# Kernel tuning notes

Hardware: AMD Instinct MI355X
Metric: run time of the kernel (lower is better)

Reference implementation:

```python
import jax, jax.numpy as jnp
import numpy as np

N_NODES = 100000

def setup_inputs() -> dict:
    key = jax.random.key(0)
    ks = jax.random.split(key, 8)
    n_feat, nhid, nclass = 256, 128, 40
    n_edges = 1600000
    x = jax.random.normal(ks[0], (N_NODES, n_feat), dtype=jnp.float32)
    edge_index = jax.random.randint(ks[1], (2, n_edges), 0, N_NODES, dtype=jnp.int64)
    # Glorot-ish scaled weights
    W1 = jax.random.normal(ks[2], (n_feat, nhid), dtype=jnp.float32) / np.sqrt(n_feat)
    b1 = jnp.zeros((nhid,), dtype=jnp.float32)
    W2 = jax.random.normal(ks[3], (nhid, nhid), dtype=jnp.float32) / np.sqrt(nhid)
    b2 = jnp.zeros((nhid,), dtype=jnp.float32)
    Wc = jax.random.normal(ks[4], (nhid, nclass), dtype=jnp.float32) / np.sqrt(nhid)
    bc = jnp.zeros((nclass,), dtype=jnp.float32)
    return {"x": x, "edge_index": edge_index, "W1": W1, "b1": b1,
            "W2": W2, "b2": b2, "Wc": Wc, "bc": bc}


def _gcn_conv(x, src, dst, W, b, n_nodes):
    """PyG GCNConv: transform, then sym-normalized aggregation with self-loops.
    out_i = sum_{j in N(i) u {i}} (d_i^-1/2 d_j^-1/2) (x_j W) + b,
    where d = in-degree over A + I.
    """
    h = x @ W  # [N, out]
    ones = jnp.ones_like(dst, dtype=h.dtype)
    deg = jax.ops.segment_sum(ones, dst, num_segments=n_nodes) + 1.0  # + self loop
    dinv = jax.lax.rsqrt(deg)  # deg >= 1, always valid
    norm = dinv[src] * dinv[dst]  # [E]
    msg = h[src] * norm[:, None]  # [E, out]  (dominant gather traffic)
    agg = jax.ops.segment_sum(msg, dst, num_segments=n_nodes)
    agg = agg + h * (dinv * dinv)[:, None]  # self-loop contribution
    return agg + b


def reference(x, edge_index, W1, b1, W2, b2, Wc, bc):
    # eval mode: dropout is identity
    src, dst = edge_index[0], edge_index[1]
    n = x.shape[0]
    h = jax.nn.relu(_gcn_conv(x, src, dst, W1, b1, n))
    h = jax.nn.relu(_gcn_conv(h, src, dst, W2, b2, n))
    return h @ Wc + bc
```

## Files before the change

### kernel.cpp

```cpp
#include <hip/hip_runtime.h>
#include <hip/hip_bf16.h>
#include <hip/hip_fp16.h>
#include <type_traits>


typedef _Float16 half8 __attribute__((ext_vector_type(8)));
typedef _Float16 half4v __attribute__((ext_vector_type(4)));
typedef float floatx4 __attribute__((ext_vector_type(4)));

#define EPB 8192


__device__ inline int block_incl_scan_256(int t, int* tmp) {
    int tid = threadIdx.x;
    tmp[tid] = t;
    __syncthreads();
    #pragma unroll
    for (int off = 1; off < 256; off <<= 1) {
        int v = (tid >= off) ? tmp[tid - off] : 0;
        __syncthreads();
        tmp[tid] += v;
        __syncthreads();
    }
    return tmp[tid];
}

template <int ITEMS>
__global__ __launch_bounds__(256) void k_scan1(const int* __restrict__ v,
                                               int* __restrict__ bsum, int n) {
    __shared__ int tmp[256];
    int base = blockIdx.x * (256 * ITEMS) + threadIdx.x * ITEMS;
    int t = 0;
    #pragma unroll
    for (int l = 0; l < ITEMS; ++l) {
        int i = base + l;
        t += (i < n) ? v[i] : 0;
    }
    block_incl_scan_256(t, tmp);
    if (threadIdx.x == 0) bsum[blockIdx.x] = tmp[255];
}

__global__ __launch_bounds__(256) void k_scan2(int* __restrict__ bsum, int nb) {
    __shared__ int tmp[256];
    int tid = threadIdx.x;
    int v = (tid < nb) ? bsum[tid] : 0;
    block_incl_scan_256(v, tmp);
    if (tid < nb) bsum[tid] = tid ? tmp[tid - 1] : 0;
}

template <int ITEMS>
__global__ __launch_bounds__(256) void k_scan3(const int* __restrict__ vin,
                                               const int* __restrict__ bsum,
                                               int* __restrict__ rp, int n) {
    __shared__ int tmp[256];
    int base = blockIdx.x * (256 * ITEMS) + threadIdx.x * ITEMS;
    int v[ITEMS];
    int t = 0;
    #pragma unroll
    for (int l = 0; l < ITEMS; ++l) {
        int i = base + l;
        v[l] = (i < n) ? vin[i] : 0;
        t += v[l];
    }
    block_incl_scan_256(t, tmp);
    int run = bsum[blockIdx.x] + (threadIdx.x ? tmp[threadIdx.x - 1] : 0);
    #pragma unroll
    for (int l = 0; l < ITEMS; ++l) {
        int i = base + l;
        if (i < n) rp[i] = run;
        run += v[l];
    }
}


__global__ __launch_bounds__(256) void k_histA(const int* __restrict__ dst,
                                               int* __restrict__ histM,
                                               int E, int nblk) {
    __shared__ int h[512];
    int tid = threadIdx.x;
    for (int i = tid; i < 512; i += 256) h[i] = 0;
    __syncthreads();
    int base = blockIdx.x * EPB;
    #pragma unroll 4
    for (int l = 0; l < EPB / 256; ++l) {
        int i = base + l * 256 + tid;
        if (i < E) atomicAdd(&h[dst[i] >> 8], 1);
    }
    __syncthreads();
    for (int i = tid; i < 512; i += 256)
        histM[i * nblk + blockIdx.x] = h[i];
}

__global__ __launch_bounds__(256) void k_scatterA(const int* __restrict__ src,
                                                  const int* __restrict__ dst,
                                                  const int* __restrict__ histS,
                                                  unsigned long long* __restrict__ eB,
                                                  int E, int nblk) {
    __shared__ int bse[512];
    __shared__ int cnt[512];
    int tid = threadIdx.x;
    for (int i = tid; i < 512; i += 256) {
        bse[i] = histS[i * nblk + blockIdx.x];
        cnt[i] = 0;
    }
    __syncthreads();
    int base = blockIdx.x * EPB;
    #pragma unroll 4
    for (int l = 0; l < EPB / 256; ++l) {
        int i = base + l * 256 + tid;
        if (i < E) {
            int d = dst[i];
            int s = src[i];
            int b = d >> 8;
            int r = atomicAdd(&cnt[b], 1);
            eB[bse[b] + r] = ((unsigned long long)(unsigned)d << 32) | (unsigned)s;
        }
    }
}

#define BCAP 4608
__global__ __launch_bounds__(256) void k_sortB(const unsigned long long* __restrict__ eB,
                                               const int* __restrict__ histS,
                                               int* __restrict__ srcS,
                                               int* __restrict__ rowptr,
                                               float* __restrict__ dinv,
                                               int n, int E, int nblk) {
    const int b   = blockIdx.x;
    const int tid = threadIdx.x;
    const int ni0 = b << 8;
    int s0 = histS[b * nblk];
    int s1 = (b < 511) ? histS[(b + 1) * nblk] : E;
    int cnt = s1 - s0;
    if (cnt > BCAP) cnt = BCAP;
    if (cnt == 0 && ni0 > n) return;

    __shared__ int hist[256];
    __shared__ int tmp[256];
    __shared__ int baseA[256];
    __shared__ int cntA[256];
    __shared__ int dstL[BCAP];
    __shared__ unsigned srcL[BCAP];
    __shared__ int lbA[256];

    hist[tid] = 0;
    cntA[tid] = 0;
    __syncthreads();
    for (int i = s0 + tid; i < s0 + cnt; i += 256) {
        int d = (int)(eB[i] >> 32);
        atomicAdd(&hist[d & 255], 1);
    }
    __syncthreads();
    int own  = hist[tid];
    int incl = block_incl_scan_256(own, tmp);
    baseA[tid] = incl - own;
    __syncthreads();
    for (int i = s0 + tid; i < s0 + cnt; i += 256) {
        unsigned long long v = eB[i];
        int d = (int)(v >> 32);
        int dig = d & 255;
        int r = atomicAdd(&cntA[dig], 1);
        int pos = baseA[dig] + r;
        dstL[pos] = d;
        srcL[pos] = (unsigned)v;
    }
    __syncthreads();
    for (int j = tid; j < cnt; j += 256)
        srcS[s0 + j] = (int)srcL[j];
    if (ni0 <= n) {
        int i = ni0 + tid;
        int lo = 0, hi = cnt;
        while (lo < hi) {
            int mid = (lo + hi) >> 1;
            if (dstL[mid] < i) lo = mid + 1; else hi = mid;
        }
        lbA[tid] = lo;
        __syncthreads();
        if (i <= n) {
            rowptr[i] = s0 + lo;
            if (i < n) {
                int ub = (tid < 255) ? lbA[tid + 1] : cnt;
                dinv[i] = rsqrtf((float)(ub - lo + 1));
            }
        }
    }
}

__global__ __launch_bounds__(256) void k_wcast(const float* __restrict__ W,
                                               _Float16* __restrict__ Wt,
                                               int N, int K, int kbits, int total) {
    int i = blockIdx.x * 256 + threadIdx.x;
    if (i < total) {
        int c = i >> kbits;
        int k = i & (K - 1);
        Wt[i] = (c < N) ? (_Float16)W[(size_t)k * N + c] : (_Float16)0.f;
    }
}


template <int K, int BN, int MT, typename AT, typename OT>
__global__ __launch_bounds__(256) void gemm_bres(const AT* __restrict__ A,
                                                 const _Float16* __restrict__ Wt,
                                                 const float* __restrict__ bias,
                                                 OT* __restrict__ C,
                                                 int M, int N) {
    constexpr int KP = K + 8;
    constexpr int NT = BN / 16;
    __shared__ __align__(16) _Float16 Bs[BN * KP];

    const int tid  = threadIdx.x;
    const int lane = tid & 63;
    const int wv   = tid >> 6;
    const int qd   = lane >> 4;
    const int ln15 = lane & 15;
    const int bm   = blockIdx.x * (64 * MT);

    constexpr int TOT = BN * K / 8;
    for (int i = tid; i < TOT; i += 256) {
        int idx = i * 8;
        int col = idx / K;
        int kk  = idx % K;
        *(uint4*)&Bs[col * KP + kk] = *(const uint4*)(Wt + idx);
    }
    __syncthreads();

    floatx4 acc[MT][NT];
    #pragma unroll
    for (int mt = 0; mt < MT; ++mt)
        #pragma unroll
        for (int c = 0; c < NT; ++c) acc[mt][c] = (floatx4){0.f, 0.f, 0.f, 0.f};

    int rw[MT];
    #pragma unroll
    for (int mt = 0; mt < MT; ++mt) {
        int r = bm + (wv * MT + mt) * 16 + ln15;
        rw[mt] = (r < M) ? r : (M - 1);
    }

    #pragma unroll
    for (int ks = 0; ks < K / 32; ++ks) {
        half8 a[MT];
        #pragma unroll
        for (int mt = 0; mt < MT; ++mt) {
            if constexpr (std::is_same<AT, float>::value) {
                const float* p = A + (size_t)rw[mt] * K + ks * 32 + qd * 8;
                float4 v0 = *(const float4*)p;
                float4 v1 = *(const float4*)(p + 4);
                half8 h;
                h[0] = (_Float16)v0.x; h[1] = (_Float16)v0.y;
                h[2] = (_Float16)v0.z; h[3] = (_Float16)v0.w;
                h[4] = (_Float16)v1.x; h[5] = (_Float16)v1.y;
                h[6] = (_Float16)v1.z; h[7] = (_Float16)v1.w;
                a[mt] = h;
            } else {
                a[mt] = *(const half8*)((const _Float16*)A +
                                        (size_t)rw[mt] * K + ks * 32 + qd * 8);
            }
        }
        #pragma unroll
        for (int c = 0; c < NT; ++c) {
            half8 b = *(const half8*)&Bs[(c * 16 + ln15) * KP + ks * 32 + qd * 8];
            #pragma unroll
            for (int mt = 0; mt < MT; ++mt)
                acc[mt][c] = __builtin_amdgcn_mfma_f32_16x16x32_f16(a[mt], b,
                                                                    acc[mt][c], 0, 0, 0);
        }
    }

    #pragma unroll
    for (int mt = 0; mt < MT; ++mt) {
        int baseRow = bm + (wv * MT + mt) * 16 + qd * 4;
        #pragma unroll
        for (int c = 0; c < NT; ++c) {
            int col = c * 16 + ln15;
            if constexpr (std::is_same<OT, _Float16>::value) {
                #pragma unroll
                for (int r = 0; r < 4; ++r) {
                    int row = baseRow + r;
                    if (row < M) C[(size_t)row * N + col] = (_Float16)acc[mt][c][r];
                }
            } else {
                float bv = (col < N && bias) ? bias[col] : 0.f;
                #pragma unroll
                for (int r = 0; r < 4; ++r) {
                    int row = baseRow + r;
                    if (row < M && col < N)
                        ((float*)C)[(size_t)row * N + col] = acc[mt][c][r] + bv;
                }
            }
        }
    }
}


__global__ __launch_bounds__(256) void gcn_agg(const unsigned int* __restrict__ h,
                                               const int* __restrict__ rowptr,
                                               const int* __restrict__ srcS,
                                               const float* __restrict__ dinv,
                                               const float* __restrict__ bias,
                                               unsigned int* __restrict__ out,
                                               int n, int do_relu) {
    int node = blockIdx.x * 4 + (threadIdx.x >> 6);
    if (node >= n) return;
    const int lane = threadIdx.x & 63;
    const int g    = lane >> 4;
    const int t    = lane & 15;

    const _Float16* hb = (const _Float16*)h;

    float di = dinv[node];
    int e0 = rowptr[node];
    int e1 = rowptr[node + 1];

    half8 sv = *(const half8*)(hb + (size_t)(unsigned)node * 128 + t * 8);
    const float4* b4 = (const float4*)bias;
    float4 blo = b4[t * 2 + 0];
    float4 bhi = b4[t * 2 + 1];

    float acc[8];
    #pragma unroll
    for (int i = 0; i < 8; ++i) acc[i] = 0.f;

    for (int ce = e0; ce < e1; ce += 64) {
        int cnt = e1 - ce;
        cnt = (cnt < 64) ? cnt : 64;
        int colv = 0, wval = 0;
        if (lane < cnt) {
            int c = srcS[ce + lane];
            colv = c;
            wval = __float_as_int(di * dinv[c]);
        }
        int d = 0;
        for (; d + 16 <= cnt; d += 16) {
            int i0 = (d + 0 + g) << 2;
            int i1 = (d + 4 + g) << 2;
            int i2 = (d + 8 + g) << 2;
            int i3 = (d + 12 + g) << 2;
            int c0 = __builtin_amdgcn_ds_bpermute(i0, colv);
            int c1 = __builtin_amdgcn_ds_bpermute(i1, colv);
            int c2 = __builtin_amdgcn_ds_bpermute(i2, colv);
            int c3 = __builtin_amdgcn_ds_bpermute(i3, colv);
            int w0i = __builtin_amdgcn_ds_bpermute(i0, wval);
            int w1i = __builtin_amdgcn_ds_bpermute(i1, wval);
            int w2i = __builtin_amdgcn_ds_bpermute(i2, wval);
            int w3i = __builtin_amdgcn_ds_bpermute(i3, wval);
            half8 h0 = *(const half8*)(hb + (size_t)(unsigned)c0 * 128 + t * 8);
            half8 h1 = *(const half8*)(hb + (size_t)(unsigned)c1 * 128 + t * 8);
            half8 h2 = *(const half8*)(hb + (size_t)(unsigned)c2 * 128 + t * 8);
            half8 h3 = *(const half8*)(hb + (size_t)(unsigned)c3 * 128 + t * 8);
            float w0 = __int_as_float(w0i);
            float w1 = __int_as_float(w1i);
            float w2 = __int_as_float(w2i);
            float w3 = __int_as_float(w3i);
            #pragma unroll
            for (int i = 0; i < 8; ++i) acc[i] += (float)h0[i] * w0;
            #pragma unroll
            for (int i = 0; i < 8; ++i) acc[i] += (float)h1[i] * w1;
            #pragma unroll
            for (int i = 0; i < 8; ++i) acc[i] += (float)h2[i] * w2;
            #pragma unroll
            for (int i = 0; i < 8; ++i) acc[i] += (float)h3[i] * w3;
        }
        for (; d < cnt; d += 4) {
            int idx = (d + g) << 2;
            int c   = __builtin_amdgcn_ds_bpermute(idx, colv);
            float w = __int_as_float(__builtin_amdgcn_ds_bpermute(idx, wval));
            half8 hv = *(const half8*)(hb + (size_t)(unsigned)c * 128 + t * 8);
            #pragma unroll
            for (int i = 0; i < 8; ++i)
                acc[i] += (float)hv[i] * w;
        }
    }

    #pragma unroll
    for (int i = 0; i < 8; ++i) acc[i] += __shfl_xor(acc[i], 16);
    #pragma unroll
    for (int i = 0; i < 8; ++i) acc[i] += __shfl_xor(acc[i], 32);

    float s = di * di;
    float bb[8] = {blo.x, blo.y, blo.z, blo.w, bhi.x, bhi.y, bhi.z, bhi.w};
    half8 o;
    #pragma unroll
    for (int i = 0; i < 8; ++i) {
        float v = acc[i] + (float)sv[i] * s + bb[i];
        if (do_relu) v = fmaxf(v, 0.f);
        o[i] = (_Float16)v;
    }
    if (g == 0)
        *(half8*)((_Float16*)out + (size_t)(unsigned)node * 128 + t * 8) = o;
}


extern "C" void kernel_launch(void* const* d_in, const int* in_sizes, int n_in,
                              void* d_out, int out_size, void* d_ws, size_t ws_size,
                              hipStream_t stream) {
    const float* x  = (const float*)d_in[0];
    const int* eidx = (const int*)d_in[1];
    const float* W1 = (const float*)d_in[2];
    const float* b1 = (const float*)d_in[3];
    const float* W2 = (const float*)d_in[4];
    const float* b2 = (const float*)d_in[5];
    const float* Wc = (const float*)d_in[6];
    const float* bc = (const float*)d_in[7];
    float* out = (float*)d_out;

    const int NF = 256, NH = 128, NC = 40;
    const int n = in_sizes[0] / NF;
    const int E = in_sizes[1] / 2;
    const int* src = eidx;
    const int* dst = eidx + E;

    const int nblk = (E + EPB - 1) / EPB;
    const int hm   = 512 * nblk;
    const int nbA  = (hm + 4095) / 4096;

    char* wsb = (char*)d_ws;
    size_t off = 0;
    auto alloc = [&](size_t bytes) {
        char* p = wsb + off;
        off = (off + bytes + 511) & ~(size_t)511;
        return p;
    };
    _Float16* hbuf = (_Float16*)alloc((size_t)n * NH * 2);
    _Float16* abuf = (_Float16*)alloc((size_t)n * NH * 2);
    _Float16* W1t  = (_Float16*)alloc((size_t)128 * 256 * 2);
    _Float16* W2t  = (_Float16*)alloc((size_t)128 * 128 * 2);
    _Float16* Wct  = (_Float16*)alloc((size_t)48 * 128 * 2);
    unsigned long long* eB = (unsigned long long*)alloc((size_t)E * 8);
    int* srcS      = (int*)alloc((size_t)E * 4);
    int* histM     = (int*)alloc((size_t)hm * 4);
    int* histS     = (int*)alloc((size_t)hm * 4);
    int* rowptr    = (int*)alloc((size_t)(n + 1) * 4);
    float* dinv    = (float*)alloc((size_t)n * 4);
    int* bsumA     = (int*)alloc(1024);

    k_histA<<<nblk, 256, 0, stream>>>(dst, histM, E, nblk);
    k_scan1<16><<<nbA, 256, 0, stream>>>(histM, bsumA, hm);
    k_scan2<<<1, 256, 0, stream>>>(bsumA, nbA);
    k_scan3<16><<<nbA, 256, 0, stream>>>(histM, bsumA, histS, hm);
    k_scatterA<<<nblk, 256, 0, stream>>>(src, dst, histS, eB, E, nblk);
    k_sortB<<<512, 256, 0, stream>>>(eB, histS, srcS, rowptr, dinv, n, E, nblk);

    k_wcast<<<(128 * 256 + 255) / 256, 256, 0, stream>>>(W1, W1t, 128, 256, 8, 128 * 256);
    k_wcast<<<(128 * 128 + 255) / 256, 256, 0, stream>>>(W2, W2t, 128, 128, 7, 128 * 128);
    k_wcast<<<(48 * 128 + 255) / 256, 256, 0, stream>>>(Wc, Wct, 40, 128, 7, 48 * 128);

    const int gB = (n + 127) / 128;
    gemm_bres<256, 128, 2, float, _Float16><<<gB, 256, 0, stream>>>(x, W1t, nullptr, hbuf, n, NH);
    gcn_agg<<<(n + 3) / 4, 256, 0, stream>>>((const unsigned int*)hbuf, rowptr, srcS, dinv, b1,
                                             (unsigned int*)abuf, n, 1);
    gemm_bres<128, 128, 2, _Float16, _Float16><<<gB, 256, 0, stream>>>(abuf, W2t, nullptr, hbuf, n, NH);
    gcn_agg<<<(n + 3) / 4, 256, 0, stream>>>((const unsigned int*)hbuf, rowptr, srcS, dinv, b2,
                                             (unsigned int*)abuf, n, 1);
    gemm_bres<128, 48, 2, _Float16, float><<<gB, 256, 0, stream>>>(abuf, Wct, bc, out, n, NC);
}
```

Before: 421.0 us.

## Store features in column-sliced layout and aggregate per slice

```diff
diff --git a/kernel.cpp b/kernel.cpp
--- a/kernel.cpp
+++ b/kernel.cpp
@@ -7,6 +7,7 @@
 typedef _Float16 half8 __attribute__((ext_vector_type(8)));
 typedef _Float16 half4v __attribute__((ext_vector_type(4)));
 typedef float floatx4 __attribute__((ext_vector_type(4)));
+typedef unsigned int uint4v __attribute__((ext_vector_type(4)));
 
 #define EPB 8192
 
@@ -197,7 +198,7 @@
 }
 
 
-template <int K, int BN, int MT, typename AT, typename OT>
+template <int K, int BN, int MT, bool BIN, bool BOUT, typename AT, typename OT>
 __global__ __launch_bounds__(256) void gemm_bres(const AT* __restrict__ A,
                                                  const _Float16* __restrict__ Wt,
                                                  const float* __restrict__ bias,
@@ -251,6 +252,11 @@
                 h[4] = (_Float16)v1.x; h[5] = (_Float16)v1.y;
                 h[6] = (_Float16)v1.z; h[7] = (_Float16)v1.w;
                 a[mt] = h;
+            } else if constexpr (BIN) {
+                int coff = ks * 32 + qd * 8;
+                const _Float16* ap = (const _Float16*)A +
+                    ((size_t)(coff >> 4) * M + rw[mt]) * 16 + (coff & 15);
+                a[mt] = *(const half8*)ap;
             } else {
                 a[mt] = *(const half8*)((const _Float16*)A +
                                         (size_t)rw[mt] * K + ks * 32 + qd * 8);
@@ -276,7 +282,13 @@
                 #pragma unroll
                 for (int r = 0; r < 4; ++r) {
                     int row = baseRow + r;
-                    if (row < M) C[(size_t)row * N + col] = (_Float16)acc[mt][c][r];
+                    if (row < M) {
+                        if constexpr (BOUT) {
+                            C[((size_t)c * M + row) * 16 + ln15] = (_Float16)acc[mt][c][r];
+                        } else {
+                            C[(size_t)row * N + col] = (_Float16)acc[mt][c][r];
+                        }
+                    }
                 }
             } else {
                 float bv = (col < N && bias) ? bias[col] : 0.f;
@@ -292,101 +304,76 @@
 }
 
 
-__global__ __launch_bounds__(256) void gcn_agg(const unsigned int* __restrict__ h,
-                                               const int* __restrict__ rowptr,
-                                               const int* __restrict__ srcS,
-                                               const float* __restrict__ dinv,
-                                               const float* __restrict__ bias,
-                                               unsigned int* __restrict__ out,
-                                               int n, int do_relu) {
-    int node = blockIdx.x * 4 + (threadIdx.x >> 6);
-    if (node >= n) return;
+__global__ __launch_bounds__(256) void gcn_agg_s(const _Float16* __restrict__ hb,
+                                                 const int* __restrict__ rowptr,
+                                                 const int* __restrict__ srcS,
+                                                 const float* __restrict__ dinv,
+                                                 const float* __restrict__ bias,
+                                                 _Float16* __restrict__ outb,
+                                                 int n, int do_relu) {
+    const int s    = blockIdx.x & 7;
+    const int g    = blockIdx.x >> 3;
+    const int wv   = threadIdx.x >> 6;
     const int lane = threadIdx.x & 63;
-    const int g    = lane >> 4;
-    const int t    = lane & 15;
-
-    const _Float16* hb = (const _Float16*)h;
-
-    float di = dinv[node];
-    int e0 = rowptr[node];
-    int e1 = rowptr[node + 1];
-
-    half8 sv = *(const half8*)(hb + (size_t)(unsigned)node * 128 + t * 8);
+    const int p    = lane >> 1;
+    const int half = lane & 1;
+    const int node = g * 128 + wv * 32 + p;
+
+    const _Float16* hs = hb + (size_t)s * n * 16;
+
+    int r0 = 0, r1 = 0;
+    float di = 0.f;
+    if (node < n) {
+        r0 = rowptr[node];
+        r1 = rowptr[node + 1];
+        di = dinv[node];
+    }
+
     const float4* b4 = (const float4*)bias;
-    float4 blo = b4[t * 2 + 0];
-    float4 bhi = b4[t * 2 + 1];
+    float4 blo = b4[s * 4 + half * 2];
+    float4 bhi = b4[s * 4 + half * 2 + 1];
 
     float acc[8];
     #pragma unroll
     for (int i = 0; i < 8; ++i) acc[i] = 0.f;
 
-    for (int ce = e0; ce < e1; ce += 64) {
-        int cnt = e1 - ce;
-        cnt = (cnt < 64) ? cnt : 64;
-        int colv = 0, wval = 0;
-        if (lane < cnt) {
-            int c = srcS[ce + lane];
-            colv = c;
-            wval = __float_as_int(di * dinv[c]);
-        }
-        int d = 0;
-        for (; d + 16 <= cnt; d += 16) {
-            int i0 = (d + 0 + g) << 2;
-            int i1 = (d + 4 + g) << 2;
-            int i2 = (d + 8 + g) << 2;
-            int i3 = (d + 12 + g) << 2;
-            int c0 = __builtin_amdgcn_ds_bpermute(i0, colv);
-            int c1 = __builtin_amdgcn_ds_bpermute(i1, colv);
-            int c2 = __builtin_amdgcn_ds_bpermute(i2, colv);
-            int c3 = __builtin_amdgcn_ds_bpermute(i3, colv);
-            int w0i = __builtin_amdgcn_ds_bpermute(i0, wval);
-            int w1i = __builtin_amdgcn_ds_bpermute(i1, wval);
-            int w2i = __builtin_amdgcn_ds_bpermute(i2, wval);
-            int w3i = __builtin_amdgcn_ds_bpermute(i3, wval);
-            half8 h0 = *(const half8*)(hb + (size_t)(unsigned)c0 * 128 + t * 8);
-            half8 h1 = *(const half8*)(hb + (size_t)(unsigned)c1 * 128 + t * 8);
-            half8 h2 = *(const half8*)(hb + (size_t)(unsigned)c2 * 128 + t * 8);
-            half8 h3 = *(const half8*)(hb + (size_t)(unsigned)c3 * 128 + t * 8);
-            float w0 = __int_as_float(w0i);
-            float w1 = __int_as_float(w1i);
-            float w2 = __int_as_float(w2i);
-            float w3 = __int_as_float(w3i);
-            #pragma unroll
-            for (int i = 0; i < 8; ++i) acc[i] += (float)h0[i] * w0;
-            #pragma unroll
-            for (int i = 0; i < 8; ++i) acc[i] += (float)h1[i] * w1;
-            #pragma unroll
-            for (int i = 0; i < 8; ++i) acc[i] += (float)h2[i] * w2;
-            #pragma unroll
-            for (int i = 0; i < 8; ++i) acc[i] += (float)h3[i] * w3;
-        }
-        for (; d < cnt; d += 4) {
-            int idx = (d + g) << 2;
-            int c   = __builtin_amdgcn_ds_bpermute(idx, colv);
-            float w = __int_as_float(__builtin_amdgcn_ds_bpermute(idx, wval));
-            half8 hv = *(const half8*)(hb + (size_t)(unsigned)c * 128 + t * 8);
-            #pragma unroll
-            for (int i = 0; i < 8; ++i)
-                acc[i] += (float)hv[i] * w;
-        }
-    }
-
-    #pragma unroll
-    for (int i = 0; i < 8; ++i) acc[i] += __shfl_xor(acc[i], 16);
-    #pragma unroll
-    for (int i = 0; i < 8; ++i) acc[i] += __shfl_xor(acc[i], 32);
-
-    float s = di * di;
-    float bb[8] = {blo.x, blo.y, blo.z, blo.w, bhi.x, bhi.y, bhi.z, bhi.w};
-    half8 o;
-    #pragma unroll
-    for (int i = 0; i < 8; ++i) {
-        float v = acc[i] + (float)sv[i] * s + bb[i];
-        if (do_relu) v = fmaxf(v, 0.f);
-        o[i] = (_Float16)v;
-    }
-    if (g == 0)
-        *(half8*)((_Float16*)out + (size_t)(unsigned)node * 128 + t * 8) = o;
+    int e = r0;
+    int c = 0;
+    float w = 0.f;
+    if (e < r1) {
+        c = __builtin_nontemporal_load(srcS + e);
+        w = di * dinv[c];
+    }
+    while (__any(e < r1)) {
+        int cc = c;
+        float cw = w;
+        ++e;
+        c = 0;
+        w = 0.f;
+        if (e < r1) {
+            c = __builtin_nontemporal_load(srcS + e);
+            w = di * dinv[c];
+        }
+        half8 hv = *(const half8*)(hs + (size_t)(unsigned)cc * 16 + half * 8);
+        #pragma unroll
+        for (int i = 0; i < 8; ++i)
+            acc[i] += (float)hv[i] * cw;
+    }
+
+    if (node < n) {
+        half8 sv = *(const half8*)(hs + (size_t)node * 16 + half * 8);
+        float sc = di * di;
+        float bb[8] = {blo.x, blo.y, blo.z, blo.w, bhi.x, bhi.y, bhi.z, bhi.w};
+        half8 o;
+        #pragma unroll
+        for (int i = 0; i < 8; ++i) {
+            float v = acc[i] + (float)sv[i] * sc + bb[i];
+            if (do_relu) v = fmaxf(v, 0.f);
+            o[i] = (_Float16)v;
+        }
+        uint4v* dst = (uint4v*)(outb + (size_t)s * n * 16 + (size_t)node * 16 + half * 8);
+        __builtin_nontemporal_store(*(uint4v*)&o, dst);
+    }
 }
 
 
@@ -444,12 +431,14 @@
     k_wcast<<<(128 * 128 + 255) / 256, 256, 0, stream>>>(W2, W2t, 128, 128, 7, 128 * 128);
     k_wcast<<<(48 * 128 + 255) / 256, 256, 0, stream>>>(Wc, Wct, 40, 128, 7, 48 * 128);
 
-    const int gB = (n + 127) / 128;
-    gemm_bres<256, 128, 2, float, _Float16><<<gB, 256, 0, stream>>>(x, W1t, nullptr, hbuf, n, NH);
-    gcn_agg<<<(n + 3) / 4, 256, 0, stream>>>((const unsigned int*)hbuf, rowptr, srcS, dinv, b1,
-                                             (unsigned int*)abuf, n, 1);
-    gemm_bres<128, 128, 2, _Float16, _Float16><<<gB, 256, 0, stream>>>(abuf, W2t, nullptr, hbuf, n, NH);
-    gcn_agg<<<(n + 3) / 4, 256, 0, stream>>>((const unsigned int*)hbuf, rowptr, srcS, dinv, b2,
-                                             (unsigned int*)abuf, n, 1);
-    gemm_bres<128, 48, 2, _Float16, float><<<gB, 256, 0, stream>>>(abuf, Wct, bc, out, n, NC);
-}
+    const int gB  = (n + 127) / 128;
+    const int gAg = ((n + 127) / 128) * 8;
+    gemm_bres<256, 128, 2, false, true, float, _Float16>
+        <<<gB, 256, 0, stream>>>(x, W1t, nullptr, hbuf, n, NH);
+    gcn_agg_s<<<gAg, 256, 0, stream>>>(hbuf, rowptr, srcS, dinv, b1, abuf, n, 1);
+    gemm_bres<128, 128, 2, true, true, _Float16, _Float16>
+        <<<gB, 256, 0, stream>>>(abuf, W2t, nullptr, hbuf, n, NH);
+    gcn_agg_s<<<gAg, 256, 0, stream>>>(hbuf, rowptr, srcS, dinv, b2, abuf, n, 1);
+    gemm_bres<128, 48, 2, true, false, _Float16, float>
+        <<<gB, 256, 0, stream>>>(abuf, Wct, bc, out, n, NC);
+}
```

Result: slower. 849.3 us (+101.7%).
